# Kernel optimization log

Measured on AMD Instinct MI355X. Metric: run time of the kernel, lower is better.

Reference implementation:

```python
import jax, jax.numpy as jnp
import numpy as np
from jax import lax

DIM = 256
NUM_HEADS = 8
HEAD_DIM = DIM // NUM_HEADS  # 32
SCALE = HEAD_DIM ** -0.5
KERNEL_SIZES = [5, 7, 9]
DILATIONS = [1, 2, 3]
# 'favor_small' allocation: weights ~ 1/k^2 over remain=num_heads-num_ranges=5
# -> extra=[3,2,0] -> heads_per_range = [4, 3, 1]
HEADS_PER_RANGE = [4, 3, 1]
B, H, W = 2, 64, 64


def setup_inputs() -> dict:
    key = jax.random.key(0)
    ks = jax.random.split(key, 9)
    d = {"x": jax.random.normal(ks[0], (B, DIM, H, W), jnp.float32)}
    for i in range(3):
        d[f"qkv_w{i}"] = jax.random.normal(ks[1 + 2 * i], (3 * DIM, DIM), jnp.float32) * 0.02
        d[f"qkv_b{i}"] = jnp.zeros((3 * DIM,), jnp.float32)
    d["proj_w"] = jax.random.normal(ks[7], (DIM, DIM), jnp.float32) * 0.02
    d["proj_b"] = jnp.zeros((DIM,), jnp.float32)
    return d


def _unfold(x, ksz, dil, h, hd):
    # x: (B, h*hd, H, W) -> (B, h, hd, L, H*W), zero-padded like F.unfold
    b, _, hh, ww = x.shape
    p = (ksz // 2) * dil
    patches = lax.conv_general_dilated_patches(
        x, (ksz, ksz), (1, 1), [(p, p), (p, p)], rhs_dilation=(dil, dil)
    )  # (B, h*hd*L, H, W), channel-major ordering matches F.unfold
    return patches.reshape(b, h, hd, ksz * ksz, hh * ww)


def _forward(x, qkv_params, proj_w, proj_b):
    b, c, hh, ww = x.shape
    hw = hh * ww
    outs = []
    hs = 0
    for i in range(len(KERNEL_SIZES)):
        w_i, b_i = qkv_params[i]
        # 1x1 conv -> qkv
        qkv = jnp.einsum('bchw,oc->bohw', x, w_i) + b_i[None, :, None, None]
        q, k, v = jnp.split(qkv, 3, axis=1)
        h_i = HEADS_PER_RANGE[i]
        he = hs + h_i
        # slice this range's heads
        q_r = q.reshape(b, NUM_HEADS, HEAD_DIM, hh, ww)[:, hs:he]
        k_r = k.reshape(b, NUM_HEADS, HEAD_DIM, hh, ww)[:, hs:he]
        v_r = v.reshape(b, NUM_HEADS, HEAD_DIM, hh, ww)[:, hs:he]
        ksz, dil = KERNEL_SIZES[i], DILATIONS[i]
        k_nb = _unfold(k_r.reshape(b, h_i * HEAD_DIM, hh, ww), ksz, dil, h_i, HEAD_DIM)
        v_nb = _unfold(v_r.reshape(b, h_i * HEAD_DIM, hh, ww), ksz, dil, h_i, HEAD_DIM)
        q_flat = q_r.reshape(b, h_i, HEAD_DIM, hw) * SCALE
        logits = jnp.einsum('bhdp,bhdlp->bhlp', q_flat, k_nb)  # (B, h_i, L, HW)
        attn = jax.nn.softmax(logits, axis=2)
        out_i = jnp.einsum('bhlp,bhdlp->bhdp', attn, v_nb)  # (B, h_i, d, HW)
        outs.append(out_i)
        hs = he
    out = jnp.concatenate(outs, axis=1).reshape(b, c, hh, ww)
    out = jnp.einsum('bchw,oc->bohw', out, proj_w) + proj_b[None, :, None, None]
    return out


def reference(x, qkv_w0, qkv_b0, qkv_w1, qkv_b1, qkv_w2, qkv_b2, proj_w, proj_b):
    qkv_params = [(qkv_w0, qkv_b0), (qkv_w1, qkv_b1), (qkv_w2, qkv_b2)]
    return _forward(x, qkv_params, proj_w, proj_b)
```

## Files before the change

### kernel.cpp

```cpp
#include <hip/hip_runtime.h>
#include <hip/hip_bf16.h>
#include <stdint.h>
#include <stddef.h>

typedef short bf16x8 __attribute__((ext_vector_type(8)));
typedef short s16x8 __attribute__((ext_vector_type(8)));
typedef float f32x4 __attribute__((ext_vector_type(4)));

#define HW 4096
#define WDIM 64

__device__ __forceinline__ short f2bf(float f) {
  union { __hip_bfloat16 b; short s; } u;
  u.b = __float2bfloat16(f);
  return u.s;
}
__device__ __forceinline__ float bf2f(short s) {
  union { unsigned u; float f; } u;
  u.u = ((unsigned)(unsigned short)s) << 16;
  return u.f;
}

__global__ void prep_weights(const float* __restrict__ w0, const float* __restrict__ w1,
                             const float* __restrict__ w2, const float* __restrict__ b0,
                             const float* __restrict__ b1, const float* __restrict__ b2,
                             const float* __restrict__ pw,
                             short* __restrict__ Wh, short* __restrict__ Wl,
                             short* __restrict__ Ph, short* __restrict__ Pl,
                             float* __restrict__ bias_sel) {
  int idx = blockIdx.x * 256 + threadIdx.x;
  if (idx < 768 * 256) {
    int j = idx >> 8;
    int h = (j & 255) >> 5;
    const float* w = (h < 4) ? w0 : ((h < 7) ? w1 : w2);
    float v = w[idx];
    short hi = f2bf(v);
    Wh[idx] = hi;
    Wl[idx] = f2bf(v - bf2f(hi));
  } else if (idx < 768 * 256 + 256 * 256) {
    int k = idx - 768 * 256;
    float v = pw[k];
    short hi = f2bf(v);
    Ph[k] = hi;
    Pl[k] = f2bf(v - bf2f(hi));
  } else if (idx < 768 * 256 + 256 * 256 + 768) {
    int j = idx - (768 * 256 + 256 * 256);
    int h = (j & 255) >> 5;
    const float* bb = (h < 4) ? b0 : ((h < 7) ? b1 : b2);
    bias_sel[j] = bb[j];
  }
}

__global__ void transpose_x(const float* __restrict__ x, short* __restrict__ XTh,
                            short* __restrict__ XTl) {
  __shared__ float tile[32][33];
  int b = blockIdx.z;
  int p0 = blockIdx.x * 32, c0 = blockIdx.y * 32;
  int tx = threadIdx.x, ty = threadIdx.y;
  const float* xb = x + (size_t)b * 256 * HW;
  #pragma unroll
  for (int i = 0; i < 32; i += 8)
    tile[ty + i][tx] = xb[(size_t)(c0 + ty + i) * HW + p0 + tx];
  __syncthreads();
  size_t ob = (size_t)b * HW * 256;
  #pragma unroll
  for (int i = 0; i < 32; i += 8) {
    float v = tile[tx][ty + i];
    short hi = f2bf(v);
    size_t o = ob + (size_t)(p0 + ty + i) * 256 + c0 + tx;
    XTh[o] = hi;
    XTl[o] = f2bf(v - bf2f(hi));
  }
}

template <int OUT>
__global__ __launch_bounds__(256) void gemm_split(
    const short* __restrict__ Ah, const short* __restrict__ Al,
    const short* __restrict__ Bh, const short* __restrict__ Bl,
    const float* __restrict__ bias, float* __restrict__ C, int M) {
  constexpr int LD = 40;
  __shared__ short Ash[128 * LD], Asl[128 * LD], Bsh[128 * LD], Bsl[128 * LD];
  int tid = threadIdx.x;
  int b = blockIdx.z;
  size_t aoff = (size_t)blockIdx.y * 128 * 256;
  size_t boff = (size_t)b * HW * 256 + (size_t)blockIdx.x * 128 * 256;
  int lane = tid & 63, wid = tid >> 6;
  int wm = wid >> 1, wn = wid & 1;
  int il = lane & 15, kg = lane >> 4;
  f32x4 acc[4][4] = {};
  int row_s = tid >> 2;
  int kk_s = (tid & 3) * 8;

  for (int kt = 0; kt < 256; kt += 32) {
    size_t ga0 = aoff + (size_t)row_s * 256 + kt + kk_s;
    size_t ga1 = aoff + (size_t)(row_s + 64) * 256 + kt + kk_s;
    size_t gb0 = boff + (size_t)row_s * 256 + kt + kk_s;
    size_t gb1 = boff + (size_t)(row_s + 64) * 256 + kt + kk_s;
    bf16x8 rah0 = *(const bf16x8*)&Ah[ga0];
    bf16x8 rah1 = *(const bf16x8*)&Ah[ga1];
    bf16x8 ral0 = *(const bf16x8*)&Al[ga0];
    bf16x8 ral1 = *(const bf16x8*)&Al[ga1];
    bf16x8 rbh0 = *(const bf16x8*)&Bh[gb0];
    bf16x8 rbh1 = *(const bf16x8*)&Bh[gb1];
    bf16x8 rbl0 = *(const bf16x8*)&Bl[gb0];
    bf16x8 rbl1 = *(const bf16x8*)&Bl[gb1];
    __syncthreads();
    *(bf16x8*)&Ash[row_s * LD + kk_s] = rah0;
    *(bf16x8*)&Ash[(row_s + 64) * LD + kk_s] = rah1;
    *(bf16x8*)&Asl[row_s * LD + kk_s] = ral0;
    *(bf16x8*)&Asl[(row_s + 64) * LD + kk_s] = ral1;
    *(bf16x8*)&Bsh[row_s * LD + kk_s] = rbh0;
    *(bf16x8*)&Bsh[(row_s + 64) * LD + kk_s] = rbh1;
    *(bf16x8*)&Bsl[row_s * LD + kk_s] = rbl0;
    *(bf16x8*)&Bsl[(row_s + 64) * LD + kk_s] = rbl1;
    __syncthreads();
    bf16x8 afh[4], afl[4], bfh[4], bfl[4];
    #pragma unroll
    for (int mr = 0; mr < 4; ++mr) {
      int r = (wm * 64 + mr * 16 + il) * LD + kg * 8;
      afh[mr] = *(bf16x8*)&Ash[r];
      afl[mr] = *(bf16x8*)&Asl[r];
    }
    #pragma unroll
    for (int nr = 0; nr < 4; ++nr) {
      int r = (wn * 64 + nr * 16 + il) * LD + kg * 8;
      bfh[nr] = *(bf16x8*)&Bsh[r];
      bfl[nr] = *(bf16x8*)&Bsl[r];
    }
    #pragma unroll
    for (int mr = 0; mr < 4; ++mr)
      #pragma unroll
      for (int nr = 0; nr < 4; ++nr) {
        acc[mr][nr] = __builtin_amdgcn_mfma_f32_16x16x32_bf16(afh[mr], bfh[nr], acc[mr][nr], 0, 0, 0);
        acc[mr][nr] = __builtin_amdgcn_mfma_f32_16x16x32_bf16(afh[mr], bfl[nr], acc[mr][nr], 0, 0, 0);
        acc[mr][nr] = __builtin_amdgcn_mfma_f32_16x16x32_bf16(afl[mr], bfh[nr], acc[mr][nr], 0, 0, 0);
      }
  }

  int m0 = blockIdx.y * 128, n0 = blockIdx.x * 128;
  #pragma unroll
  for (int mr = 0; mr < 4; ++mr) {
    #pragma unroll
    for (int nr = 0; nr < 4; ++nr) {
      int grow0 = m0 + wm * 64 + mr * 16 + kg * 4;
      int gcol = n0 + wn * 64 + nr * 16 + il;
      if (OUT == 0) {
        int t = grow0 >> 8, h = (grow0 >> 5) & 7, d0 = grow0 & 31;
        size_t base = (((size_t)(b * 3 + t) * 8 + h) << 17) + ((size_t)gcol << 5) + d0;
        f32x4 vv;
        #pragma unroll
        for (int r = 0; r < 4; ++r) vv[r] = acc[mr][nr][r] + bias[grow0 + r];
        *(f32x4*)&C[base] = vv;
      } else {
        size_t cbase = (size_t)b * M * HW;
        #pragma unroll
        for (int r = 0; r < 4; ++r)
          C[cbase + (size_t)(grow0 + r) * HW + gcol] = acc[mr][nr][r] + bias[grow0 + r];
      }
    }
  }
}

template <int KSZ, int DIL>
__device__ __forceinline__ void attn_wave(const float* __restrict__ qkvt,
                                          short* __restrict__ Yh, short* __restrict__ Yl,
                                          int b, int hq, int p0, int lane) {
  constexpr int R = KSZ / 2;
  const float SCALE = 0.17677669529663687f;
  int pl = lane & 15;
  int dq = lane >> 4;
  int p = p0 + pl;
  const float* qrow = qkvt + (((size_t)(b * 24 + hq)) << 17) + ((size_t)p << 5) + dq * 8;
  const float* kb = qkvt + (((size_t)(b * 24 + 8 + hq)) << 17) + dq * 8;
  const float* vb = qkvt + (((size_t)(b * 24 + 16 + hq)) << 17) + dq * 8;

  f32x4 q0 = *(const f32x4*)&qrow[0];
  f32x4 q1 = *(const f32x4*)&qrow[4];
  #pragma unroll
  for (int j = 0; j < 4; ++j) { q0[j] *= SCALE; q1[j] *= SCALE; }

  f32x4 a0 = {0.f, 0.f, 0.f, 0.f}, a1 = {0.f, 0.f, 0.f, 0.f};
  float denom = 0.f;
  int y = p >> 6, x = p & 63;

  #pragma unroll
  for (int dy = -R; dy <= R; ++dy) {
    int ny = y + dy * DIL;
    #pragma unroll
    for (int dx = -R; dx <= R; ++dx) {
      int nx = x + dx * DIL;
      if ((unsigned)ny < WDIM && (unsigned)nx < WDIM) {
        int pp = ny * WDIM + nx;
        const float* krow = kb + ((size_t)pp << 5);
        f32x4 k0 = *(const f32x4*)&krow[0];
        f32x4 k1 = *(const f32x4*)&krow[4];
        float s = q0[0] * k0[0] + q0[1] * k0[1] + q0[2] * k0[2] + q0[3] * k0[3]
                + q1[0] * k1[0] + q1[1] * k1[1] + q1[2] * k1[2] + q1[3] * k1[3];
        s += __shfl_xor(s, 16);
        s += __shfl_xor(s, 32);
        float e = __expf(s);
        denom += e;
        const float* vrow = vb + ((size_t)pp << 5);
        f32x4 v0 = *(const f32x4*)&vrow[0];
        f32x4 v1 = *(const f32x4*)&vrow[4];
        #pragma unroll
        for (int j = 0; j < 4; ++j) { a0[j] += e * v0[j]; a1[j] += e * v1[j]; }
      } else {
        denom += 1.0f;
      }
    }
  }

  float inv = 1.0f / denom;
  size_t yo = ((size_t)b * HW + p) * 256 + hq * 32 + dq * 8;
  s16x8 oh, ol;
  #pragma unroll
  for (int j = 0; j < 4; ++j) {
    float v = a0[j] * inv;
    short hi = f2bf(v);
    oh[j] = hi; ol[j] = f2bf(v - bf2f(hi));
    float w = a1[j] * inv;
    short hi2 = f2bf(w);
    oh[4 + j] = hi2; ol[4 + j] = f2bf(w - bf2f(hi2));
  }
  *(s16x8*)&Yh[yo] = oh;
  *(s16x8*)&Yl[yo] = ol;
}

__global__ __launch_bounds__(256, 8) void attn_all(const float* __restrict__ qkvt,
                                                   short* __restrict__ Yh,
                                                   short* __restrict__ Yl) {
  int tid = threadIdx.x;
  int lane = tid & 63, wave = tid >> 6;
  int bx = blockIdx.x;
  if (bx < 512) {
    int tile = bx & 63;
    int rest = bx >> 6;
    int b = rest & 1, h = rest >> 1;
    attn_wave<5, 1>(qkvt, Yh, Yl, b, h, tile * 64 + wave * 16, lane);
  } else if (bx < 896) {
    int s = bx - 512;
    int tile = s & 63;
    int rest = s >> 6;
    int b = rest & 1, h = 4 + (rest >> 1);
    attn_wave<7, 2>(qkvt, Yh, Yl, b, h, tile * 64 + wave * 16, lane);
  } else {
    int s = bx - 896;
    int tile = s & 63;
    int b = s >> 6;
    attn_wave<9, 3>(qkvt, Yh, Yl, b, 7, tile * 64 + wave * 16, lane);
  }
}

extern "C" void kernel_launch(void* const* d_in, const int* in_sizes, int n_in,
                              void* d_out, int out_size, void* d_ws, size_t ws_size,
                              hipStream_t stream) {
  const float* x  = (const float*)d_in[0];
  const float* w0 = (const float*)d_in[1];
  const float* b0 = (const float*)d_in[2];
  const float* w1 = (const float*)d_in[3];
  const float* b1 = (const float*)d_in[4];
  const float* w2 = (const float*)d_in[5];
  const float* b2 = (const float*)d_in[6];
  const float* pw = (const float*)d_in[7];
  const float* pb = (const float*)d_in[8];

  char* ws = (char*)d_ws;
  float* qkvt = (float*)ws; ws += (size_t)2 * 768 * HW * 4;
  short* XTh = (short*)ws;  ws += (size_t)2 * HW * 256 * 2;
  short* XTl = (short*)ws;  ws += (size_t)2 * HW * 256 * 2;
  short* Yh  = (short*)ws;  ws += (size_t)2 * HW * 256 * 2;
  short* Yl  = (short*)ws;  ws += (size_t)2 * HW * 256 * 2;
  short* Wh  = (short*)ws;  ws += (size_t)768 * 256 * 2;
  short* Wl  = (short*)ws;  ws += (size_t)768 * 256 * 2;
  short* Ph  = (short*)ws;  ws += (size_t)256 * 256 * 2;
  short* Pl  = (short*)ws;  ws += (size_t)256 * 256 * 2;
  float* bsel= (float*)ws;  ws += 4096;

  prep_weights<<<1027, 256, 0, stream>>>(w0, w1, w2, b0, b1, b2, pw, Wh, Wl, Ph, Pl, bsel);
  transpose_x<<<dim3(128, 8, 2), dim3(32, 8), 0, stream>>>(x, XTh, XTl);
  gemm_split<0><<<dim3(32, 6, 2), 256, 0, stream>>>(Wh, Wl, XTh, XTl, bsel, qkvt, 768);
  attn_all<<<1024, 256, 0, stream>>>(qkvt, Yh, Yl);
  gemm_split<1><<<dim3(32, 2, 2), 256, 0, stream>>>(Ph, Pl, Yh, Yl, pb, (float*)d_out, 256);
}
```

Measured before the change: 222.5 us.

## Shrink GEMM tiles and remap attention to 8 pixels per wave branchlessly

Templates the split-bf16 GEMM on tile sizes and launches it with smaller tiles (64x128 for QKV, 64x64 for projection), raising block counts to fill more CUs. The attention kernel now maps 8 pixels per wave with 8 lanes per head, each holding 4 dims, so twice as many waves run. Out-of-bounds neighbours are handled by clamping the load to the pixel itself and masking, which removes the branch. The cost is an extra shuffle step per neighbour and less reuse per GEMM tile.

```diff
diff --git a/kernel.cpp b/kernel.cpp
--- a/kernel.cpp
+++ b/kernel.cpp
@@ -4,7 +4,7 @@
 #include <stddef.h>
 
 typedef short bf16x8 __attribute__((ext_vector_type(8)));
-typedef short s16x8 __attribute__((ext_vector_type(8)));
+typedef short s16x4 __attribute__((ext_vector_type(4)));
 typedef float f32x4 __attribute__((ext_vector_type(4)));
 
 #define HW 4096
@@ -73,77 +73,83 @@
   }
 }
 
-template <int OUT>
+template <int BM, int BN, int OUT>
 __global__ __launch_bounds__(256) void gemm_split(
     const short* __restrict__ Ah, const short* __restrict__ Al,
     const short* __restrict__ Bh, const short* __restrict__ Bl,
     const float* __restrict__ bias, float* __restrict__ C, int M) {
   constexpr int LD = 40;
-  __shared__ short Ash[128 * LD], Asl[128 * LD], Bsh[128 * LD], Bsl[128 * LD];
+  constexpr int AL = BM / 64, BL = BN / 64;
+  constexpr int WM = BM / 2, WN = BN / 2;
+  constexpr int MR = WM / 16, NR = WN / 16;
+  __shared__ short Ash[BM * LD], Asl[BM * LD], Bsh[BN * LD], Bsl[BN * LD];
   int tid = threadIdx.x;
   int b = blockIdx.z;
-  size_t aoff = (size_t)blockIdx.y * 128 * 256;
-  size_t boff = (size_t)b * HW * 256 + (size_t)blockIdx.x * 128 * 256;
+  size_t aoff = (size_t)blockIdx.y * BM * 256;
+  size_t boff = (size_t)b * HW * 256 + (size_t)blockIdx.x * BN * 256;
   int lane = tid & 63, wid = tid >> 6;
   int wm = wid >> 1, wn = wid & 1;
   int il = lane & 15, kg = lane >> 4;
-  f32x4 acc[4][4] = {};
+  f32x4 acc[MR][NR] = {};
   int row_s = tid >> 2;
   int kk_s = (tid & 3) * 8;
 
   for (int kt = 0; kt < 256; kt += 32) {
-    size_t ga0 = aoff + (size_t)row_s * 256 + kt + kk_s;
-    size_t ga1 = aoff + (size_t)(row_s + 64) * 256 + kt + kk_s;
-    size_t gb0 = boff + (size_t)row_s * 256 + kt + kk_s;
-    size_t gb1 = boff + (size_t)(row_s + 64) * 256 + kt + kk_s;
-    bf16x8 rah0 = *(const bf16x8*)&Ah[ga0];
-    bf16x8 rah1 = *(const bf16x8*)&Ah[ga1];
-    bf16x8 ral0 = *(const bf16x8*)&Al[ga0];
-    bf16x8 ral1 = *(const bf16x8*)&Al[ga1];
-    bf16x8 rbh0 = *(const bf16x8*)&Bh[gb0];
-    bf16x8 rbh1 = *(const bf16x8*)&Bh[gb1];
-    bf16x8 rbl0 = *(const bf16x8*)&Bl[gb0];
-    bf16x8 rbl1 = *(const bf16x8*)&Bl[gb1];
+    bf16x8 rah[AL], ral[AL], rbh[BL], rbl[BL];
+    #pragma unroll
+    for (int i = 0; i < AL; ++i) {
+      size_t g = aoff + (size_t)(row_s + 64 * i) * 256 + kt + kk_s;
+      rah[i] = *(const bf16x8*)&Ah[g];
+      ral[i] = *(const bf16x8*)&Al[g];
+    }
+    #pragma unroll
+    for (int i = 0; i < BL; ++i) {
+      size_t g = boff + (size_t)(row_s + 64 * i) * 256 + kt + kk_s;
+      rbh[i] = *(const bf16x8*)&Bh[g];
+      rbl[i] = *(const bf16x8*)&Bl[g];
+    }
     __syncthreads();
-    *(bf16x8*)&Ash[row_s * LD + kk_s] = rah0;
-    *(bf16x8*)&Ash[(row_s + 64) * LD + kk_s] = rah1;
-    *(bf16x8*)&Asl[row_s * LD + kk_s] = ral0;
-    *(bf16x8*)&Asl[(row_s + 64) * LD + kk_s] = ral1;
-    *(bf16x8*)&Bsh[row_s * LD + kk_s] = rbh0;
-    *(bf16x8*)&Bsh[(row_s + 64) * LD + kk_s] = rbh1;
-    *(bf16x8*)&Bsl[row_s * LD + kk_s] = rbl0;
-    *(bf16x8*)&Bsl[(row_s + 64) * LD + kk_s] = rbl1;
+    #pragma unroll
+    for (int i = 0; i < AL; ++i) {
+      *(bf16x8*)&Ash[(row_s + 64 * i) * LD + kk_s] = rah[i];
+      *(bf16x8*)&Asl[(row_s + 64 * i) * LD + kk_s] = ral[i];
+    }
+    #pragma unroll
+    for (int i = 0; i < BL; ++i) {
+      *(bf16x8*)&Bsh[(row_s + 64 * i) * LD + kk_s] = rbh[i];
+      *(bf16x8*)&Bsl[(row_s + 64 * i) * LD + kk_s] = rbl[i];
+    }
     __syncthreads();
-    bf16x8 afh[4], afl[4], bfh[4], bfl[4];
-    #pragma unroll
-    for (int mr = 0; mr < 4; ++mr) {
-      int r = (wm * 64 + mr * 16 + il) * LD + kg * 8;
+    bf16x8 afh[MR], afl[MR], bfh[NR], bfl[NR];
+    #pragma unroll
+    for (int mr = 0; mr < MR; ++mr) {
+      int r = (wm * WM + mr * 16 + il) * LD + kg * 8;
       afh[mr] = *(bf16x8*)&Ash[r];
       afl[mr] = *(bf16x8*)&Asl[r];
     }
     #pragma unroll
-    for (int nr = 0; nr < 4; ++nr) {
-      int r = (wn * 64 + nr * 16 + il) * LD + kg * 8;
+    for (int nr = 0; nr < NR; ++nr) {
+      int r = (wn * WN + nr * 16 + il) * LD + kg * 8;
       bfh[nr] = *(bf16x8*)&Bsh[r];
       bfl[nr] = *(bf16x8*)&Bsl[r];
     }
     #pragma unroll
-    for (int mr = 0; mr < 4; ++mr)
+    for (int mr = 0; mr < MR; ++mr)
       #pragma unroll
-      for (int nr = 0; nr < 4; ++nr) {
+      for (int nr = 0; nr < NR; ++nr) {
         acc[mr][nr] = __builtin_amdgcn_mfma_f32_16x16x32_bf16(afh[mr], bfh[nr], acc[mr][nr], 0, 0, 0);
         acc[mr][nr] = __builtin_amdgcn_mfma_f32_16x16x32_bf16(afh[mr], bfl[nr], acc[mr][nr], 0, 0, 0);
         acc[mr][nr] = __builtin_amdgcn_mfma_f32_16x16x32_bf16(afl[mr], bfh[nr], acc[mr][nr], 0, 0, 0);
       }
   }
 
-  int m0 = blockIdx.y * 128, n0 = blockIdx.x * 128;
-  #pragma unroll
-  for (int mr = 0; mr < 4; ++mr) {
-    #pragma unroll
-    for (int nr = 0; nr < 4; ++nr) {
-      int grow0 = m0 + wm * 64 + mr * 16 + kg * 4;
-      int gcol = n0 + wn * 64 + nr * 16 + il;
+  int m0 = blockIdx.y * BM, n0 = blockIdx.x * BN;
+  #pragma unroll
+  for (int mr = 0; mr < MR; ++mr) {
+    #pragma unroll
+    for (int nr = 0; nr < NR; ++nr) {
+      int grow0 = m0 + wm * WM + mr * 16 + kg * 4;
+      int gcol = n0 + wn * WN + nr * 16 + il;
       if (OUT == 0) {
         int t = grow0 >> 8, h = (grow0 >> 5) & 7, d0 = grow0 & 31;
         size_t base = (((size_t)(b * 3 + t) * 8 + h) << 17) + ((size_t)gcol << 5) + d0;
@@ -167,64 +173,55 @@
                                           int b, int hq, int p0, int lane) {
   constexpr int R = KSZ / 2;
   const float SCALE = 0.17677669529663687f;
-  int pl = lane & 15;
-  int dq = lane >> 4;
+  int pl = lane & 7;
+  int dq = lane >> 3;
   int p = p0 + pl;
-  const float* qrow = qkvt + (((size_t)(b * 24 + hq)) << 17) + ((size_t)p << 5) + dq * 8;
-  const float* kb = qkvt + (((size_t)(b * 24 + 8 + hq)) << 17) + dq * 8;
-  const float* vb = qkvt + (((size_t)(b * 24 + 16 + hq)) << 17) + dq * 8;
-
-  f32x4 q0 = *(const f32x4*)&qrow[0];
-  f32x4 q1 = *(const f32x4*)&qrow[4];
-  #pragma unroll
-  for (int j = 0; j < 4; ++j) { q0[j] *= SCALE; q1[j] *= SCALE; }
-
-  f32x4 a0 = {0.f, 0.f, 0.f, 0.f}, a1 = {0.f, 0.f, 0.f, 0.f};
+  const float* qp = qkvt + (((size_t)(b * 24 + hq)) << 17) + ((size_t)p << 5) + dq * 4;
+  const float* kb = qkvt + (((size_t)(b * 24 + 8 + hq)) << 17) + dq * 4;
+  const float* vb = qkvt + (((size_t)(b * 24 + 16 + hq)) << 17) + dq * 4;
+
+  f32x4 q = *(const f32x4*)qp;
+  #pragma unroll
+  for (int j = 0; j < 4; ++j) q[j] *= SCALE;
+
+  f32x4 acc = {0.f, 0.f, 0.f, 0.f};
   float denom = 0.f;
   int y = p >> 6, x = p & 63;
 
   #pragma unroll
   for (int dy = -R; dy <= R; ++dy) {
-    int ny = y + dy * DIL;
     #pragma unroll
     for (int dx = -R; dx <= R; ++dx) {
+      int ny = y + dy * DIL;
       int nx = x + dx * DIL;
-      if ((unsigned)ny < WDIM && (unsigned)nx < WDIM) {
-        int pp = ny * WDIM + nx;
-        const float* krow = kb + ((size_t)pp << 5);
-        f32x4 k0 = *(const f32x4*)&krow[0];
-        f32x4 k1 = *(const f32x4*)&krow[4];
-        float s = q0[0] * k0[0] + q0[1] * k0[1] + q0[2] * k0[2] + q0[3] * k0[3]
-                + q1[0] * k1[0] + q1[1] * k1[1] + q1[2] * k1[2] + q1[3] * k1[3];
-        s += __shfl_xor(s, 16);
-        s += __shfl_xor(s, 32);
-        float e = __expf(s);
-        denom += e;
-        const float* vrow = vb + ((size_t)pp << 5);
-        f32x4 v0 = *(const f32x4*)&vrow[0];
-        f32x4 v1 = *(const f32x4*)&vrow[4];
-        #pragma unroll
-        for (int j = 0; j < 4; ++j) { a0[j] += e * v0[j]; a1[j] += e * v1[j]; }
-      } else {
-        denom += 1.0f;
-      }
+      bool valid = ((unsigned)ny < WDIM) & ((unsigned)nx < WDIM);
+      int pp = valid ? (ny * WDIM + nx) : p;
+      f32x4 kk = *(const f32x4*)(kb + ((size_t)pp << 5));
+      f32x4 vv = *(const f32x4*)(vb + ((size_t)pp << 5));
+      float s = q[0] * kk[0] + q[1] * kk[1] + q[2] * kk[2] + q[3] * kk[3];
+      s += __shfl_xor(s, 8);
+      s += __shfl_xor(s, 16);
+      s += __shfl_xor(s, 32);
+      float e = __expf(valid ? s : 0.0f);
+      denom += e;
+      float en = valid ? e : 0.0f;
+      #pragma unroll
+      for (int j = 0; j < 4; ++j) acc[j] += en * vv[j];
     }
   }
 
   float inv = 1.0f / denom;
-  size_t yo = ((size_t)b * HW + p) * 256 + hq * 32 + dq * 8;
-  s16x8 oh, ol;
+  size_t yo = ((size_t)b * HW + p) * 256 + hq * 32 + dq * 4;
+  s16x4 oh, ol;
   #pragma unroll
   for (int j = 0; j < 4; ++j) {
-    float v = a0[j] * inv;
-    short hi = f2bf(v);
-    oh[j] = hi; ol[j] = f2bf(v - bf2f(hi));
-    float w = a1[j] * inv;
-    short hi2 = f2bf(w);
-    oh[4 + j] = hi2; ol[4 + j] = f2bf(w - bf2f(hi2));
-  }
-  *(s16x8*)&Yh[yo] = oh;
-  *(s16x8*)&Yl[yo] = ol;
+    float v = acc[j] * inv;
+    short hi = f2bf(v);
+    oh[j] = hi;
+    ol[j] = f2bf(v - bf2f(hi));
+  }
+  *(s16x4*)&Yh[yo] = oh;
+  *(s16x4*)&Yl[yo] = ol;
 }
 
 __global__ __launch_bounds__(256, 8) void attn_all(const float* __restrict__ qkvt,
@@ -232,23 +229,23 @@
                                                    short* __restrict__ Yl) {
   int tid = threadIdx.x;
   int lane = tid & 63, wave = tid >> 6;
-  int bx = blockIdx.x;
-  if (bx < 512) {
-    int tile = bx & 63;
-    int rest = bx >> 6;
-    int b = rest & 1, h = rest >> 1;
-    attn_wave<5, 1>(qkvt, Yh, Yl, b, h, tile * 64 + wave * 16, lane);
-  } else if (bx < 896) {
-    int s = bx - 512;
-    int tile = s & 63;
-    int rest = s >> 6;
-    int b = rest & 1, h = 4 + (rest >> 1);
-    attn_wave<7, 2>(qkvt, Yh, Yl, b, h, tile * 64 + wave * 16, lane);
+  int gw = blockIdx.x * 4 + wave;
+  if (gw < 4096) {
+    int tile = gw & 511;
+    int t2 = gw >> 9;
+    int b = t2 & 1, h = t2 >> 1;
+    attn_wave<5, 1>(qkvt, Yh, Yl, b, h, tile * 8, lane);
+  } else if (gw < 7168) {
+    int s = gw - 4096;
+    int tile = s & 511;
+    int t2 = s >> 9;
+    int b = t2 & 1, h = 4 + (t2 >> 1);
+    attn_wave<7, 2>(qkvt, Yh, Yl, b, h, tile * 8, lane);
   } else {
-    int s = bx - 896;
-    int tile = s & 63;
-    int b = s >> 6;
-    attn_wave<9, 3>(qkvt, Yh, Yl, b, 7, tile * 64 + wave * 16, lane);
+    int s = gw - 7168;
+    int tile = s & 511;
+    int b = s >> 9;
+    attn_wave<9, 3>(qkvt, Yh, Yl, b, 7, tile * 8, lane);
   }
 }
 
@@ -279,7 +276,7 @@
 
   prep_weights<<<1027, 256, 0, stream>>>(w0, w1, w2, b0, b1, b2, pw, Wh, Wl, Ph, Pl, bsel);
   transpose_x<<<dim3(128, 8, 2), dim3(32, 8), 0, stream>>>(x, XTh, XTl);
-  gemm_split<0><<<dim3(32, 6, 2), 256, 0, stream>>>(Wh, Wl, XTh, XTl, bsel, qkvt, 768);
-  attn_all<<<1024, 256, 0, stream>>>(qkvt, Yh, Yl);
-  gemm_split<1><<<dim3(32, 2, 2), 256, 0, stream>>>(Ph, Pl, Yh, Yl, pb, (float*)d_out, 256);
-}
+  gemm_split<64, 128, 0><<<dim3(32, 12, 2), 256, 0, stream>>>(Wh, Wl, XTh, XTl, bsel, qkvt, 768);
+  attn_all<<<2048, 256, 0, stream>>>(qkvt, Yh, Yl);
+  gemm_split<64, 64, 1><<<dim3(64, 4, 2), 256, 0, stream>>>(Ph, Pl, Yh, Yl, pb, (float*)d_out, 256);
+}
```

Result: faster. 198.0 us (-11.0%).
